# Kernel optimization log

Hardware: AMD Instinct MI355X
Metric: run time of the kernel (lower is better)

## Reference

```python
import jax, jax.numpy as jnp
import numpy as np

B, H, K, L, V = 4096, 1024, 10, 64, 80  # batch, hidden, mixtures, char_len, vocab

def setup_inputs() -> dict:
    key = jax.random.key(0)
    k1, k2, k3, k4 = jax.random.split(key, 4)
    return {
        "x": jax.random.normal(k1, (B, H), dtype=jnp.float32),
        "chars": jax.random.normal(k2, (B, L, V), dtype=jnp.float32),
        "W": jax.random.normal(k3, (H, 3 * K), dtype=jnp.float32) * 0.02,
        "b": jax.random.normal(k4, (3 * K,), dtype=jnp.float32) * 0.02,
    }

def reference(x, chars, W, b):
    # Linear: [B, 3K]
    out = x @ W + b
    alpha_raw, beta_raw, kappa_raw = jnp.split(out, 3, axis=1)  # each [B, K]
    alpha = jnp.exp(alpha_raw)[:, :, None]            # [B, K, 1]
    beta = jnp.exp(beta_raw)[:, :, None]              # [B, K, 1]
    # kappa_prev is zero on first call -> kappa = exp(kappa_raw)
    kappa = jnp.exp(kappa_raw)[:, :, None]            # [B, K, 1]
    u = jnp.arange(L, dtype=jnp.float32)[None, None, :]  # [1, 1, L]
    phi = jnp.sum(alpha * jnp.exp(-beta * (kappa - u) ** 2), axis=1)  # [B, L]
    window = jnp.einsum('bl,blv->bv', phi, chars)     # [B, V]
    return window
```

## Files before the change

### kernel.cpp

```cpp
#include <hip/hip_runtime.h>
#include <math.h>
#include <stdint.h>

constexpr int Bn = 4096;
constexpr int Hn = 1024;
constexpr int Kn = 10;
constexpr int Ln = 64;
constexpr int Vn = 80;
constexpr int NJ = 3 * Kn;
constexpr int R  = 2;
constexpr int NT = 256;

typedef const __attribute__((address_space(1))) uint32_t glb_u32;
typedef __attribute__((address_space(3))) uint32_t lds_u32;
__device__ __forceinline__ void gload_lds16(const void* g, void* l) {
    __builtin_amdgcn_global_load_lds((glb_u32*)g, (lds_u32*)l, 16, 0, 0);
}

__global__ __launch_bounds__(NT) void window_fused(
    const float* __restrict__ x,
    const float* __restrict__ chars,
    const float* __restrict__ W,
    const float* __restrict__ bias,
    float* __restrict__ out)
{
    __shared__ float4 cs4[R * Ln * Vn / 4];
    __shared__ float4 xs4[R * Hn / 4];
    __shared__ float  red[R * 256];
    __shared__ float  abk[R * NJ];
    __shared__ float  phi_s[R * Ln];

    const int t    = threadIdx.x;
    const int lane = t & 63;
    const int w    = t >> 6;
    const int row0 = blockIdx.x * R;

    const float4* xg4 = (const float4*)(x + (size_t)row0 * Hn);
    float4 xa = xg4[t];
    float4 xb = xg4[NT + t];
    float bias_v = 0.f;
    if (t < R * NJ) bias_v = bias[t % NJ];
    xs4[t]      = xa;
    xs4[NT + t] = xb;

    const char* cg = (const char*)(chars + (size_t)row0 * Ln * Vn);
    char*       cl = (char*)cs4;
#pragma unroll
    for (int i = 0; i < 10; ++i) {
        const int off = (w * 10 + i) * 1024;
        gload_lds16(cg + off + lane * 16, cl + off);
    }

    asm volatile("s_waitcnt lgkmcnt(0)" ::: "memory");
    __builtin_amdgcn_s_barrier();
    __builtin_amdgcn_sched_barrier(0);

    const int j = t & 31;
    const int g = t >> 5;
    float acc0 = 0.f, acc1 = 0.f;
    if (j < NJ) {
        const float* Wp = W + j;
        const int h0 = g * 128;
#pragma unroll 4
        for (int ii = 0; ii < 128; ii += 4) {
            const int h  = h0 + ii;
            const int h4 = h >> 2;
            float4 va = xs4[h4];
            float4 vb = xs4[(Hn / 4) + h4];
            float w0 = Wp[(h + 0) * NJ];
            float w1 = Wp[(h + 1) * NJ];
            float w2 = Wp[(h + 2) * NJ];
            float w3 = Wp[(h + 3) * NJ];
            acc0 += w0 * va.x + w1 * va.y + w2 * va.z + w3 * va.w;
            acc1 += w0 * vb.x + w1 * vb.y + w2 * vb.z + w3 * vb.w;
        }
    }
    red[0 * 256 + g * 32 + j] = acc0;
    red[1 * 256 + g * 32 + j] = acc1;
    asm volatile("s_waitcnt lgkmcnt(0)" ::: "memory");
    __builtin_amdgcn_s_barrier();
    __builtin_amdgcn_sched_barrier(0);

    if (t < R * NJ) {
        const int r = t / NJ, jj = t % NJ;
        float s = bias_v;
#pragma unroll
        for (int gg = 0; gg < 8; ++gg) s += red[r * 256 + gg * 32 + jj];
        abk[r * NJ + jj] = __expf(s);
    }
    asm volatile("s_waitcnt lgkmcnt(0)" ::: "memory");
    __builtin_amdgcn_s_barrier();
    __builtin_amdgcn_sched_barrier(0);

    if (t < R * Ln) {
        const int r = t >> 6, l = t & 63;
        const float lf = (float)l;
        const float* ab = abk + r * NJ;
        float ph = 0.f;
#pragma unroll
        for (int k = 0; k < Kn; ++k) {
            float a  = ab[k];
            float bt = ab[Kn + k];
            float kp = ab[2 * Kn + k];
            float d  = kp - lf;
            ph += a * __expf(-bt * d * d);
        }
        phi_s[r * Ln + l] = ph;
    }

    __syncthreads();

    float4* cpart = (float4*)xs4;
    if (t < 240) {
        const int v4  = t % 20;
        const int g12 = t / 20;
        float4 s0 = make_float4(0.f, 0.f, 0.f, 0.f);
        float4 s1 = s0;
        for (int l = g12; l < Ln; l += 12) {
            float4 cA = cs4[l * 20 + v4];
            float4 cB = cs4[1280 + l * 20 + v4];
            float p0 = phi_s[l];
            float p1 = phi_s[Ln + l];
            s0.x += p0 * cA.x; s0.y += p0 * cA.y; s0.z += p0 * cA.z; s0.w += p0 * cA.w;
            s1.x += p1 * cB.x; s1.y += p1 * cB.y; s1.z += p1 * cB.z; s1.w += p1 * cB.w;
        }
        cpart[(0 * 12 + g12) * 20 + v4] = s0;
        cpart[(1 * 12 + g12) * 20 + v4] = s1;
    }
    __syncthreads();

    if (t < R * 20) {
        const int r  = t / 20;
        const int vv = t % 20;
        float4 s = make_float4(0.f, 0.f, 0.f, 0.f);
#pragma unroll
        for (int gg = 0; gg < 12; ++gg) {
            float4 p = cpart[(r * 12 + gg) * 20 + vv];
            s.x += p.x; s.y += p.y; s.z += p.z; s.w += p.w;
        }
        ((float4*)out)[(size_t)(row0 + r) * 20 + vv] = s;
    }
}

extern "C" void kernel_launch(void* const* d_in, const int* in_sizes, int n_in,
                              void* d_out, int out_size, void* d_ws, size_t ws_size,
                              hipStream_t stream) {
    const float* x     = (const float*)d_in[0];
    const float* chars = (const float*)d_in[1];
    const float* W     = (const float*)d_in[2];
    const float* bias  = (const float*)d_in[3];
    float* out = (float*)d_out;

    window_fused<<<Bn / R, NT, 0, stream>>>(x, chars, W, bias, out);
}
```

Measured before the change: 148.5 us.

## Process eight rows per block with double-buffered chars streaming into LDS

Each block now handles eight batch rows instead of two, reusing each W load across all eight rows in the linear projection. The chars tiles are streamed per row through two LDS buffers with async global-to-LDS loads, so the load of the next row overlaps compute on the current one. The cost is fewer blocks (512), more serialized barriers per block, and LDS being reused for x, chars and the partial sums.

After: 150.5 us. No clear change (+1.4%).

```diff
diff --git a/kernel.cpp b/kernel.cpp
--- a/kernel.cpp
+++ b/kernel.cpp
@@ -8,7 +8,7 @@
 constexpr int Ln = 64;
 constexpr int Vn = 80;
 constexpr int NJ = 3 * Kn;
-constexpr int R  = 2;
+constexpr int R  = 8;
 constexpr int NT = 256;
 
 typedef const __attribute__((address_space(1))) uint32_t glb_u32;
@@ -16,6 +16,10 @@
 __device__ __forceinline__ void gload_lds16(const void* g, void* l) {
     __builtin_amdgcn_global_load_lds((glb_u32*)g, (lds_u32*)l, 16, 0, 0);
 }
+#define VMCNT(n) asm volatile("s_waitcnt vmcnt(" #n ")" ::: "memory")
+#define LGKM0()  asm volatile("s_waitcnt lgkmcnt(0)" ::: "memory")
+#define BAR()    __builtin_amdgcn_s_barrier()
+#define SCHED()  __builtin_amdgcn_sched_barrier(0)
 
 __global__ __launch_bounds__(NT) void window_fused(
     const float* __restrict__ x,
@@ -24,8 +28,7 @@
     const float* __restrict__ bias,
     float* __restrict__ out)
 {
-    __shared__ float4 cs4[R * Ln * Vn / 4];
-    __shared__ float4 xs4[R * Hn / 4];
+    __shared__ float4 buf[2][Ln * Vn / 4];
     __shared__ float  red[R * 256];
     __shared__ float  abk[R * NJ];
     __shared__ float  phi_s[R * Ln];
@@ -35,99 +38,122 @@
     const int w    = t >> 6;
     const int row0 = blockIdx.x * R;
 
-    const float4* xg4 = (const float4*)(x + (size_t)row0 * Hn);
-    float4 xa = xg4[t];
-    float4 xb = xg4[NT + t];
-    float bias_v = 0.f;
-    if (t < R * NJ) bias_v = bias[t % NJ];
-    xs4[t]      = xa;
-    xs4[NT + t] = xb;
-
-    const char* cg = (const char*)(chars + (size_t)row0 * Ln * Vn);
-    char*       cl = (char*)cs4;
+    {
+        const char* xg = (const char*)(x + (size_t)row0 * Hn);
+        char*       bl = (char*)buf;
 #pragma unroll
-    for (int i = 0; i < 10; ++i) {
-        const int off = (w * 10 + i) * 1024;
-        gload_lds16(cg + off + lane * 16, cl + off);
-    }
-
-    asm volatile("s_waitcnt lgkmcnt(0)" ::: "memory");
-    __builtin_amdgcn_s_barrier();
-    __builtin_amdgcn_sched_barrier(0);
-
-    const int j = t & 31;
-    const int g = t >> 5;
-    float acc0 = 0.f, acc1 = 0.f;
-    if (j < NJ) {
-        const float* Wp = W + j;
-        const int h0 = g * 128;
-#pragma unroll 4
-        for (int ii = 0; ii < 128; ii += 4) {
-            const int h  = h0 + ii;
-            const int h4 = h >> 2;
-            float4 va = xs4[h4];
-            float4 vb = xs4[(Hn / 4) + h4];
-            float w0 = Wp[(h + 0) * NJ];
-            float w1 = Wp[(h + 1) * NJ];
-            float w2 = Wp[(h + 2) * NJ];
-            float w3 = Wp[(h + 3) * NJ];
-            acc0 += w0 * va.x + w1 * va.y + w2 * va.z + w3 * va.w;
-            acc1 += w0 * vb.x + w1 * vb.y + w2 * vb.z + w3 * vb.w;
+        for (int i = 0; i < 8; ++i) {
+            const int off = (w * 8 + i) * 1024;
+            gload_lds16(xg + off + lane * 16, bl + off);
         }
     }
-    red[0 * 256 + g * 32 + j] = acc0;
-    red[1 * 256 + g * 32 + j] = acc1;
-    asm volatile("s_waitcnt lgkmcnt(0)" ::: "memory");
-    __builtin_amdgcn_s_barrier();
-    __builtin_amdgcn_sched_barrier(0);
+    VMCNT(0); BAR(); SCHED();
+
+    {
+        const float4* xs4 = (const float4*)buf;
+        const int j = t & 31;
+        const int g = t >> 5;
+        float acc[R];
+#pragma unroll
+        for (int r = 0; r < R; ++r) acc[r] = 0.f;
+        if (j < NJ) {
+            const float* Wp = W + j;
+            const int h0 = g * 128;
+#pragma unroll 4
+            for (int ii = 0; ii < 128; ii += 4) {
+                const int h  = h0 + ii;
+                const int h4 = h >> 2;
+                float w0 = Wp[(h + 0) * NJ];
+                float w1 = Wp[(h + 1) * NJ];
+                float w2 = Wp[(h + 2) * NJ];
+                float w3 = Wp[(h + 3) * NJ];
+#pragma unroll
+                for (int r = 0; r < R; ++r) {
+                    float4 v = xs4[r * 256 + h4];
+                    acc[r] += w0 * v.x + w1 * v.y + w2 * v.z + w3 * v.w;
+                }
+            }
+        }
+#pragma unroll
+        for (int r = 0; r < R; ++r) red[r * 256 + g * 32 + j] = acc[r];
+    }
+    LGKM0(); BAR(); SCHED();
 
     if (t < R * NJ) {
         const int r = t / NJ, jj = t % NJ;
-        float s = bias_v;
+        float s = bias[jj];
 #pragma unroll
         for (int gg = 0; gg < 8; ++gg) s += red[r * 256 + gg * 32 + jj];
         abk[r * NJ + jj] = __expf(s);
     }
-    asm volatile("s_waitcnt lgkmcnt(0)" ::: "memory");
-    __builtin_amdgcn_s_barrier();
-    __builtin_amdgcn_sched_barrier(0);
+    LGKM0(); BAR(); SCHED();
 
-    if (t < R * Ln) {
-        const int r = t >> 6, l = t & 63;
+    const char* cg = (const char*)(chars + (size_t)row0 * Ln * Vn);
+    VMCNT(0);
+#define ISSUE(gi, bsel)                                                     \
+    {                                                                       \
+        const char* src = cg + (gi) * 20480;                                \
+        char*       dst = (char*)(buf[(bsel)]);                             \
+        _Pragma("unroll")                                                   \
+        for (int c2 = 0; c2 < 5; ++c2) {             \
+            const int off = (w * 5 + c2) * 1024;                            \
+            gload_lds16(src + off + lane * 16, dst + off);                  \
+        }                                                                   \
+    }
+    ISSUE(0, 0);
+    ISSUE(1, 1);
+
+    {
+        const int l = t & 63;
         const float lf = (float)l;
-        const float* ab = abk + r * NJ;
-        float ph = 0.f;
 #pragma unroll
-        for (int k = 0; k < Kn; ++k) {
-            float a  = ab[k];
-            float bt = ab[Kn + k];
-            float kp = ab[2 * Kn + k];
-            float d  = kp - lf;
-            ph += a * __expf(-bt * d * d);
+        for (int rr = 0; rr < 2; ++rr) {
+            const int r = (t >> 6) + rr * 4;
+            const float* ab = abk + r * NJ;
+            float ph = 0.f;
+#pragma unroll
+            for (int k = 0; k < Kn; ++k) {
+                float a  = ab[k];
+                float bt = ab[Kn + k];
+                float kp = ab[2 * Kn + k];
+                float d  = kp - lf;
+                ph += a * __expf(-bt * d * d);
+            }
+            phi_s[r * Ln + l] = ph;
         }
-        phi_s[r * Ln + l] = ph;
+    }
+    LGKM0(); BAR(); SCHED();
+
+    const int v4 = t % 20;
+    const int lg = t / 20;
+    float4 eacc[R];
+#pragma unroll
+    for (int i = 0; i < R; ++i) eacc[i] = make_float4(0.f, 0.f, 0.f, 0.f);
+
+#pragma unroll
+    for (int i = 0; i < R; ++i) {
+        if (i < R - 1) { VMCNT(5); } else { VMCNT(0); }
+        BAR(); SCHED();
+        if (t < 240) {
+            const float4* cs = (const float4*)(buf[i & 1]);
+            float4 a = eacc[i];
+            for (int l = lg; l < Ln; l += 12) {
+                float4 c = cs[l * 20 + v4];
+                float  p = phi_s[i * Ln + l];
+                a.x += p * c.x; a.y += p * c.y; a.z += p * c.z; a.w += p * c.w;
+            }
+            eacc[i] = a;
+        }
+        LGKM0(); BAR(); SCHED();
+        if (i + 2 < R) ISSUE(i + 2, i & 1);
     }
 
-    __syncthreads();
-
-    float4* cpart = (float4*)xs4;
+    float4* cpart = (float4*)buf;
     if (t < 240) {
-        const int v4  = t % 20;
-        const int g12 = t / 20;
-        float4 s0 = make_float4(0.f, 0.f, 0.f, 0.f);
-        float4 s1 = s0;
-        for (int l = g12; l < Ln; l += 12) {
-            float4 cA = cs4[l * 20 + v4];
-            float4 cB = cs4[1280 + l * 20 + v4];
-            float p0 = phi_s[l];
-            float p1 = phi_s[Ln + l];
-            s0.x += p0 * cA.x; s0.y += p0 * cA.y; s0.z += p0 * cA.z; s0.w += p0 * cA.w;
-            s1.x += p1 * cB.x; s1.y += p1 * cB.y; s1.z += p1 * cB.z; s1.w += p1 * cB.w;
-        }
-        cpart[(0 * 12 + g12) * 20 + v4] = s0;
-        cpart[(1 * 12 + g12) * 20 + v4] = s1;
+#pragma unroll
+        for (int i = 0; i < R; ++i) cpart[i * 240 + t] = eacc[i];
     }
-    __syncthreads();
+    LGKM0(); BAR(); SCHED();
 
     if (t < R * 20) {
         const int r  = t / 20;
@@ -135,7 +161,7 @@
         float4 s = make_float4(0.f, 0.f, 0.f, 0.f);
 #pragma unroll
         for (int gg = 0; gg < 12; ++gg) {
-            float4 p = cpart[(r * 12 + gg) * 20 + vv];
+            float4 p = cpart[r * 240 + gg * 20 + vv];
             s.x += p.x; s.y += p.y; s.z += p.z; s.w += p.w;
         }
         ((float4*)out)[(size_t)(row0 + r) * 20 + vv] = s;
```

## Hold chars tiles in registers, process four rows per block, shuffle-reduce window

Applied to the files above, without the earlier changes.

The chars tile is no longer staged in LDS through global_load_lds. Each thread now loads its 16 float4 slices directly into registers, and the final L-reduction runs across 4 lanes with xor shuffles instead of an LDS partial-sum pass. Rows per block go from 2 to 4 and threads from 256 to 320, so each W load is reused across four rows, and the W loads become float2 with a padded partial-sum layout. The intent is to cut LDS traffic, free LDS for occupancy, and amortize W reads. The cost is higher register pressure from 64 floats of chars per thread and fewer blocks overall.

New measurement: 158.1 us. +6.5%, slower.

```diff
diff --git a/kernel.cpp b/kernel.cpp
--- a/kernel.cpp
+++ b/kernel.cpp
@@ -1,6 +1,5 @@
 #include <hip/hip_runtime.h>
 #include <math.h>
-#include <stdint.h>
 
 constexpr int Bn = 4096;
 constexpr int Hn = 1024;
@@ -8,14 +7,9 @@
 constexpr int Ln = 64;
 constexpr int Vn = 80;
 constexpr int NJ = 3 * Kn;
-constexpr int R  = 2;
-constexpr int NT = 256;
-
-typedef const __attribute__((address_space(1))) uint32_t glb_u32;
-typedef __attribute__((address_space(3))) uint32_t lds_u32;
-__device__ __forceinline__ void gload_lds16(const void* g, void* l) {
-    __builtin_amdgcn_global_load_lds((glb_u32*)g, (lds_u32*)l, 16, 0, 0);
-}
+constexpr int R  = 4;
+constexpr int NT = 320;
+constexpr int PJ = 17;
 
 __global__ __launch_bounds__(NT) void window_fused(
     const float* __restrict__ x,
@@ -24,78 +18,85 @@
     const float* __restrict__ bias,
     float* __restrict__ out)
 {
-    __shared__ float4 cs4[R * Ln * Vn / 4];
     __shared__ float4 xs4[R * Hn / 4];
-    __shared__ float  red[R * 256];
+    __shared__ float  part[R * 512];
     __shared__ float  abk[R * NJ];
     __shared__ float  phi_s[R * Ln];
 
     const int t    = threadIdx.x;
-    const int lane = t & 63;
-    const int w    = t >> 6;
     const int row0 = blockIdx.x * R;
 
-    const float4* xg4 = (const float4*)(x + (size_t)row0 * Hn);
-    float4 xa = xg4[t];
-    float4 xb = xg4[NT + t];
+    const int q  = t & 3;
+    const int v4 = (t >> 2) % 20;
+    const int rr = t / 80;
+
+    float4 xa, xb, xc, xd;
+    if (t < 256) {
+        const float4* xg4 = (const float4*)(x + (size_t)row0 * Hn);
+        xa = xg4[t]; xb = xg4[256 + t]; xc = xg4[512 + t]; xd = xg4[768 + t];
+    }
     float bias_v = 0.f;
     if (t < R * NJ) bias_v = bias[t % NJ];
-    xs4[t]      = xa;
-    xs4[NT + t] = xb;
 
-    const char* cg = (const char*)(chars + (size_t)row0 * Ln * Vn);
-    char*       cl = (char*)cs4;
+    float4 c[16];
+    {
+        const float4* cb = (const float4*)chars
+                         + (size_t)(row0 + rr) * 1280
+                         + q * 320 + v4;
 #pragma unroll
-    for (int i = 0; i < 10; ++i) {
-        const int off = (w * 10 + i) * 1024;
-        gload_lds16(cg + off + lane * 16, cl + off);
+        for (int i = 0; i < 16; ++i) c[i] = cb[i * 20];
     }
 
-    asm volatile("s_waitcnt lgkmcnt(0)" ::: "memory");
-    __builtin_amdgcn_s_barrier();
-    __builtin_amdgcn_sched_barrier(0);
+    if (t < 256) {
+        xs4[t] = xa; xs4[256 + t] = xb; xs4[512 + t] = xc; xs4[768 + t] = xd;
+    }
+    __syncthreads();
 
-    const int j = t & 31;
-    const int g = t >> 5;
-    float acc0 = 0.f, acc1 = 0.f;
-    if (j < NJ) {
-        const float* Wp = W + j;
-        const int h0 = g * 128;
+    {
+        const int jp = t & 15;
+        const int g  = t >> 4;
+        if (t < 256 && jp < 15) {
+            const float* W2 = W + 2 * jp;
+            float aA[R], aB[R];
+#pragma unroll
+            for (int r0 = 0; r0 < R; ++r0) { aA[r0] = 0.f; aB[r0] = 0.f; }
+            const int h0 = g * 64;
 #pragma unroll 4
-        for (int ii = 0; ii < 128; ii += 4) {
-            const int h  = h0 + ii;
-            const int h4 = h >> 2;
-            float4 va = xs4[h4];
-            float4 vb = xs4[(Hn / 4) + h4];
-            float w0 = Wp[(h + 0) * NJ];
-            float w1 = Wp[(h + 1) * NJ];
-            float w2 = Wp[(h + 2) * NJ];
-            float w3 = Wp[(h + 3) * NJ];
-            acc0 += w0 * va.x + w1 * va.y + w2 * va.z + w3 * va.w;
-            acc1 += w0 * vb.x + w1 * vb.y + w2 * vb.z + w3 * vb.w;
+            for (int ii = 0; ii < 64; ii += 4) {
+                const int h = h0 + ii;
+                float2 w0 = *(const float2*)(W2 + (h + 0) * NJ);
+                float2 w1 = *(const float2*)(W2 + (h + 1) * NJ);
+                float2 w2 = *(const float2*)(W2 + (h + 2) * NJ);
+                float2 w3 = *(const float2*)(W2 + (h + 3) * NJ);
+#pragma unroll
+                for (int r0 = 0; r0 < R; ++r0) {
+                    float4 xv = xs4[r0 * 256 + (h >> 2)];
+                    aA[r0] += w0.x * xv.x + w1.x * xv.y + w2.x * xv.z + w3.x * xv.w;
+                    aB[r0] += w0.y * xv.x + w1.y * xv.y + w2.y * xv.z + w3.y * xv.w;
+                }
+            }
+#pragma unroll
+            for (int r0 = 0; r0 < R; ++r0) {
+                part[r0 * 512 + (2 * jp + 0) * PJ + g] = aA[r0];
+                part[r0 * 512 + (2 * jp + 1) * PJ + g] = aB[r0];
+            }
         }
     }
-    red[0 * 256 + g * 32 + j] = acc0;
-    red[1 * 256 + g * 32 + j] = acc1;
-    asm volatile("s_waitcnt lgkmcnt(0)" ::: "memory");
-    __builtin_amdgcn_s_barrier();
-    __builtin_amdgcn_sched_barrier(0);
+    __syncthreads();
 
     if (t < R * NJ) {
-        const int r = t / NJ, jj = t % NJ;
+        const int r0 = t / NJ, j = t % NJ;
         float s = bias_v;
 #pragma unroll
-        for (int gg = 0; gg < 8; ++gg) s += red[r * 256 + gg * 32 + jj];
-        abk[r * NJ + jj] = __expf(s);
+        for (int gg = 0; gg < 16; ++gg) s += part[r0 * 512 + j * PJ + gg];
+        abk[r0 * NJ + j] = __expf(s);
     }
-    asm volatile("s_waitcnt lgkmcnt(0)" ::: "memory");
-    __builtin_amdgcn_s_barrier();
-    __builtin_amdgcn_sched_barrier(0);
+    __syncthreads();
 
-    if (t < R * Ln) {
-        const int r = t >> 6, l = t & 63;
+    if (t < 256) {
+        const int r0 = t >> 6, l = t & 63;
         const float lf = (float)l;
-        const float* ab = abk + r * NJ;
+        const float* ab = abk + r0 * NJ;
         float ph = 0.f;
 #pragma unroll
         for (int k = 0; k < Kn; ++k) {
@@ -105,41 +106,25 @@
             float d  = kp - lf;
             ph += a * __expf(-bt * d * d);
         }
-        phi_s[r * Ln + l] = ph;
-    }
-
-    __syncthreads();
-
-    float4* cpart = (float4*)xs4;
-    if (t < 240) {
-        const int v4  = t % 20;
-        const int g12 = t / 20;
-        float4 s0 = make_float4(0.f, 0.f, 0.f, 0.f);
-        float4 s1 = s0;
-        for (int l = g12; l < Ln; l += 12) {
-            float4 cA = cs4[l * 20 + v4];
-            float4 cB = cs4[1280 + l * 20 + v4];
-            float p0 = phi_s[l];
-            float p1 = phi_s[Ln + l];
-            s0.x += p0 * cA.x; s0.y += p0 * cA.y; s0.z += p0 * cA.z; s0.w += p0 * cA.w;
-            s1.x += p1 * cB.x; s1.y += p1 * cB.y; s1.z += p1 * cB.z; s1.w += p1 * cB.w;
-        }
-        cpart[(0 * 12 + g12) * 20 + v4] = s0;
-        cpart[(1 * 12 + g12) * 20 + v4] = s1;
+        phi_s[r0 * Ln + l] = ph;
     }
     __syncthreads();
 
-    if (t < R * 20) {
-        const int r  = t / 20;
-        const int vv = t % 20;
-        float4 s = make_float4(0.f, 0.f, 0.f, 0.f);
+    float4 s = make_float4(0.f, 0.f, 0.f, 0.f);
+    const float* ph = phi_s + rr * Ln + q * 16;
 #pragma unroll
-        for (int gg = 0; gg < 12; ++gg) {
-            float4 p = cpart[(r * 12 + gg) * 20 + vv];
-            s.x += p.x; s.y += p.y; s.z += p.z; s.w += p.w;
-        }
-        ((float4*)out)[(size_t)(row0 + r) * 20 + vv] = s;
+    for (int i = 0; i < 16; ++i) {
+        float p = ph[i];
+        s.x += p * c[i].x; s.y += p * c[i].y;
+        s.z += p * c[i].z; s.w += p * c[i].w;
     }
+    s.x += __shfl_xor(s.x, 1); s.y += __shfl_xor(s.y, 1);
+    s.z += __shfl_xor(s.z, 1); s.w += __shfl_xor(s.w, 1);
+    s.x += __shfl_xor(s.x, 2); s.y += __shfl_xor(s.y, 2);
+    s.z += __shfl_xor(s.z, 2); s.w += __shfl_xor(s.w, 2);
+
+    if (q == 0)
+        ((float4*)out)[(size_t)(row0 + rr) * 20 + v4] = s;
 }
 
 extern "C" void kernel_launch(void* const* d_in, const int* in_sizes, int n_in,
```
